# Optimization experiments

Hardware: AMD Instinct MI355X
Metric: run time of the kernel (lower is better)

The kernel has to match this reference:

```python
import jax, jax.numpy as jnp
import numpy as np

N = 50000      # num_nodes
R = 90         # num_relations
E = 800000     # num_edges
H = 16         # hidden channels
B = 30         # num_bases
C = 8          # num_classes


def setup_inputs() -> dict:
    key = jax.random.key(0)
    ks = jax.random.split(key, 10)
    edge_index = jax.random.randint(ks[0], (2, E), 0, N, dtype=jnp.int64)
    edge_type = jax.random.randint(ks[1], (E,), 0, R, dtype=jnp.int64)
    s1 = 1.0 / np.sqrt(N)
    s2 = 1.0 / np.sqrt(H)
    return {
        "edge_index": edge_index,
        "edge_type": edge_type,
        # layer 1: in=N (featureless one-hot), out=H
        "basis1": jax.random.normal(ks[2], (B, N, H), jnp.float32) * s1,
        "comp1": jax.random.normal(ks[3], (R, B), jnp.float32) * (1.0 / np.sqrt(B)),
        "root1": jax.random.normal(ks[4], (N, H), jnp.float32) * s1,
        "bias1": jnp.zeros((H,), jnp.float32),
        # layer 2: in=H, out=C
        "basis2": jax.random.normal(ks[5], (B, H, C), jnp.float32) * s2,
        "comp2": jax.random.normal(ks[6], (R, B), jnp.float32) * (1.0 / np.sqrt(B)),
        "root2": jax.random.normal(ks[7], (H, C), jnp.float32) * s2,
        "bias2": jnp.zeros((C,), jnp.float32),
    }


def reference(edge_index, edge_type, basis1, comp1, root1, bias1,
              basis2, comp2, root2, bias2):
    src, dst = edge_index[0], edge_index[1]
    # per-(dst, relation) degree -> mean aggregation per relation (PyG RGCNConv aggr='mean')
    seg = dst * R + edge_type                      # [E]
    deg = jax.ops.segment_sum(jnp.ones((E,), jnp.float32), seg, num_segments=N * R)
    inv_deg = jnp.where(deg > 0, 1.0 / jnp.maximum(deg, 1.0), 0.0)
    norm = inv_deg[seg][:, None]                   # [E, 1]

    # ---- layer 1 (x = None -> one-hot node features; message = W_r[src]) ----
    W1 = jnp.einsum('rb,bnh->rnh', comp1, basis1)  # [R, N, H]
    m1 = W1[edge_type, src] * norm                 # [E, H]
    h = jax.ops.segment_sum(m1, dst, num_segments=N) + root1 + bias1  # [N, H]
    h = jax.nn.relu(h)

    # ---- layer 2 ----
    W2 = jnp.einsum('rb,bhc->rhc', comp2, basis2)  # [R, H, C]
    m2 = jnp.einsum('eh,ehc->ec', h[src], W2[edge_type]) * norm       # [E, C]
    out = jax.ops.segment_sum(m2, dst, num_segments=N) + h @ root2 + bias2
    return jax.nn.log_softmax(out, axis=1)
```

## Files before the change

### kernel.cpp

```cpp
#include <hip/hip_runtime.h>

#define NNODES 50000
#define NREL   90
#define NEDGE  800000
#define HDIM   16
#define NBASIS 30
#define NCLS   8
#define NPART  392
#define CH     2048
#define P1BLK  ((NEDGE + CH - 1) / CH)
#define CAPSTG 2816
#define GS     8
#define BSTR2  260
#define CROW2  20

typedef __fp16 h2 __attribute__((ext_vector_type(2)));

static __device__ __forceinline__ unsigned pk2(float a, float b) {
    h2 p = __builtin_amdgcn_cvt_pkrtz(a, b);
    return __builtin_bit_cast(unsigned, p);
}
static __device__ __forceinline__ h2 uph(unsigned u) {
    return __builtin_bit_cast(h2, u);
}
static __device__ __forceinline__ float fd2(unsigned a, unsigned b, float c) {
#if __has_builtin(__builtin_amdgcn_fdot2)
    return __builtin_amdgcn_fdot2(uph(a), uph(b), c, false);
#else
    h2 x = uph(a), y = uph(b);
    return fmaf((float)x.y, (float)y.y, fmaf((float)x.x, (float)y.x, c));
#endif
}

__device__ __forceinline__ void scan512_incl(int* sc) {
    int t = threadIdx.x;
#pragma unroll
    for (int d = 1; d < 512; d <<= 1) {
        int v0 = sc[t];
        int a0 = (t >= d) ? sc[t - d] : 0;
        int v1 = sc[t + 256];
        int a1 = sc[t + 256 - d];
        __syncthreads();
        sc[t] = v0 + a0;
        sc[t + 256] = v1 + a1;
        __syncthreads();
    }
}

__device__ __forceinline__ void scan128_incl(int* sc) {
    int t = threadIdx.x;
#pragma unroll
    for (int d = 1; d < 128; d <<= 1) {
        int v = 0, a = 0;
        if (t < 128) { v = sc[t]; a = (t >= d) ? sc[t - d] : 0; }
        __syncthreads();
        if (t < 128) sc[t] = v + a;
        __syncthreads();
    }
}

__global__ __launch_bounds__(256) void initc_kernel(int* __restrict__ gcur_s,
                                                    int* __restrict__ gcur_d,
                                                    int* __restrict__ gcnt,
                                                    const float* __restrict__ comp1,
                                                    unsigned* __restrict__ comp_pk) {
    int t = blockIdx.x * 256 + threadIdx.x;
    if (t < NPART) { gcur_s[t] = t * CAPSTG; gcur_d[t] = t * CAPSTG; }
    else if (t == NPART) { gcnt[0] = 0; gcnt[1] = 0; }
    int i = t - 512;
    if (i >= 0 && i < NREL * 15) {
        int r = i / 15;
        int b2 = i - r * 15;
        comp_pk[r * CROW2 + b2] = pk2(comp1[r * NBASIS + 2 * b2],
                                      comp1[r * NBASIS + 2 * b2 + 1]);
    }
    if (i >= NREL * 15 && i < NREL * 15 + NREL * (CROW2 - 15)) {
        int j = i - NREL * 15;
        int r = j / (CROW2 - 15);
        int pcol = 15 + (j - r * (CROW2 - 15));
        comp_pk[r * CROW2 + pcol] = 0;
    }
}

__global__ __launch_bounds__(256) void p1d_kernel(const int* __restrict__ ei,
                                                  const int* __restrict__ et,
                                                  int* __restrict__ gcur_d,
                                                  int2* __restrict__ stg_d) {
    __shared__ int2 sorted[CH];
    __shared__ int hist[NPART], loff[NPART], cur[NPART], gbase[NPART];
    __shared__ int sc[512];
    int base = blockIdx.x * CH;
    int nitems = min(CH, NEDGE - base);
    int t = threadIdx.x;
    for (int i = t; i < NPART; i += 256) hist[i] = 0;
    __syncthreads();
    for (int i = t; i < nitems; i += 256)
        atomicAdd(&hist[ei[NEDGE + base + i] >> 7], 1);
    __syncthreads();
    sc[t]       = (t < NPART) ? hist[t] : 0;
    sc[t + 256] = (t + 256 < NPART) ? hist[t + 256] : 0;
    __syncthreads();
    scan512_incl(sc);
    for (int p = t; p < NPART; p += 256) {
        int lo = p ? sc[p - 1] : 0;
        loff[p] = lo;
        cur[p] = lo;
        if (hist[p]) gbase[p] = atomicAdd(&gcur_d[p], hist[p]);
    }
    __syncthreads();
    for (int i = t; i < nitems; i += 256) {
        int e = base + i;
        int src = ei[e], dst = ei[NEDGE + e], r = et[e];
        int rk = atomicAdd(&cur[dst >> 7], 1);
        sorted[rk] = make_int2(src | (r << 16), dst);
    }
    __syncthreads();
    for (int s = t; s < nitems; s += 256) {
        int2 it = sorted[s];
        int p = it.y >> 7;
        stg_d[gbase[p] + (s - loff[p])] = it;
    }
}

__global__ __launch_bounds__(256) void p2d_kernel(const int* __restrict__ gcur_d,
                                                  const int2* __restrict__ stg_d,
                                                  int* __restrict__ gcur_s,
                                                  int2* __restrict__ stg_s,
                                                  int* __restrict__ gcnt,
                                                  int* __restrict__ d_sr,
                                                  float* __restrict__ d_norm,
                                                  int* __restrict__ offs_d,
                                                  int* __restrict__ cnt_d) {
    __shared__ int2 sorted[CAPSTG];
    __shared__ int2 sorted2[CAPSTG];
    __shared__ int h[128], off[128], cur[128];
    __shared__ int sc[512];
    __shared__ int shist[NPART], sloff[NPART], scur[NPART], sgbase[NPART];
    __shared__ int kb;
    int p = blockIdx.x;
    int base = p * CAPSTG;
    int n = min(gcur_d[p] - base, CAPSTG);
    int t = threadIdx.x;
    if (t < 128) h[t] = 0;
    __syncthreads();
    for (int s = t; s < n; s += 256)
        atomicAdd(&h[stg_d[base + s].y & 127], 1);
    __syncthreads();
    if (t < 128) sc[t] = h[t];
    __syncthreads();
    scan128_incl(sc);
    if (t < 128) { int lo = t ? sc[t - 1] : 0; off[t] = lo; cur[t] = lo; }
    if (t == 0) kb = atomicAdd(&gcnt[0], n);
    __syncthreads();
    for (int s = t; s < n; s += 256) {
        int2 it = stg_d[base + s];
        int rk = atomicAdd(&cur[it.y & 127], 1);
        sorted[rk] = it;
    }
    __syncthreads();
    int kbase = kb;
    for (int s = t; s < n; s += 256) {
        int2 it = sorted[s];
        int key = it.y & 127;
        int r = it.x >> 16;
        int o = off[key], oe = o + h[key];
        int c = 0;
        for (int kk = o; kk < oe; ++kk)
            c += ((sorted[kk].x >> 16) == r);
        d_sr[kbase + s] = it.x;
        d_norm[kbase + s] = 1.0f / (float)c;
    }
    if (t < 128) {
        int node = (p << 7) + t;
        if (node < NNODES) { offs_d[node] = kbase + off[t]; cnt_d[node] = h[t]; }
    }
    for (int i = t; i < NPART; i += 256) shist[i] = 0;
    __syncthreads();
    for (int s = t; s < n; s += 256)
        atomicAdd(&shist[(sorted[s].x & 0xFFFF) >> 7], 1);
    __syncthreads();
    sc[t]       = (t < NPART) ? shist[t] : 0;
    sc[t + 256] = (t + 256 < NPART) ? shist[t + 256] : 0;
    __syncthreads();
    scan512_incl(sc);
    for (int pp = t; pp < NPART; pp += 256) {
        int lo = pp ? sc[pp - 1] : 0;
        sloff[pp] = lo;
        scur[pp] = lo;
        if (shist[pp]) sgbase[pp] = atomicAdd(&gcur_s[pp], shist[pp]);
    }
    __syncthreads();
    for (int s = t; s < n; s += 256) {
        int2 it = sorted[s];
        int rk = atomicAdd(&scur[(it.x & 0xFFFF) >> 7], 1);
        sorted2[rk] = make_int2(it.x, kbase + s);
    }
    __syncthreads();
    for (int s = t; s < n; s += 256) {
        int2 it = sorted2[s];
        int pp = (it.x & 0xFFFF) >> 7;
        stg_s[sgbase[pp] + (s - sloff[pp])] = it;
    }
}

__global__ __launch_bounds__(256) void p2s_kernel(const int* __restrict__ gcur_s,
                                                  const int2* __restrict__ stg_s,
                                                  int* __restrict__ gcnt,
                                                  int* __restrict__ sB,
                                                  int* __restrict__ s_k,
                                                  int* __restrict__ offs_s,
                                                  int* __restrict__ cnt_s) {
    __shared__ int2 sorted[CAPSTG];
    __shared__ int h[128], off[128], cur[128], sc[128];
    __shared__ int jb;
    int p = blockIdx.x;
    int base = p * CAPSTG;
    int n = min(gcur_s[p] - base, CAPSTG);
    int t = threadIdx.x;
    if (t < 128) h[t] = 0;
    __syncthreads();
    for (int s = t; s < n; s += 256)
        atomicAdd(&h[stg_s[base + s].x & 127], 1);
    __syncthreads();
    if (t < 128) sc[t] = h[t];
    __syncthreads();
    scan128_incl(sc);
    if (t < 128) { int lo = t ? sc[t - 1] : 0; off[t] = lo; cur[t] = lo; }
    if (t == 0) jb = atomicAdd(&gcnt[1], n);
    __syncthreads();
    for (int s = t; s < n; s += 256) {
        int2 it = stg_s[base + s];
        int rk = atomicAdd(&cur[it.x & 127], 1);
        sorted[rk] = it;
    }
    __syncthreads();
    int jbase = jb;
    for (int s = t; s < n; s += 256) {
        int2 it = sorted[s];
        sB[jbase + s]  = it.x;
        s_k[jbase + s] = it.y;
    }
    if (t < 128) {
        int node = (p << 7) + t;
        if (node < NNODES) { offs_s[node] = jbase + off[t]; cnt_s[node] = h[t]; }
    }
}

__global__ __launch_bounds__(256) void msg1_lds(const float* __restrict__ basis1,
                                                const unsigned* __restrict__ comp_pk,
                                                const int* __restrict__ offs_s,
                                                const int* __restrict__ cnt_s,
                                                const int* __restrict__ sB,
                                                const int* __restrict__ s_k,
                                                unsigned* __restrict__ m1) {
    __shared__ unsigned bspk[GS * BSTR2];
    __shared__ unsigned cpk[NREL * CROW2];
    int src0 = blockIdx.x * GS;
    int t = threadIdx.x;
    for (int i = t; i < (NREL * CROW2) / 4; i += 256)
        ((uint4*)cpk)[i] = ((const uint4*)comp_pk)[i];
    for (int i4 = t; i4 < 15 * 32; i4 += 256) {
        int b2 = i4 >> 5;
        int w  = i4 & 31;
        const float4* bp = (const float4*)basis1;
        float4 a = bp[(size_t)(2 * b2)     * (NNODES * 4) + (size_t)src0 * 4 + w];
        float4 b = bp[(size_t)(2 * b2 + 1) * (NNODES * 4) + (size_t)src0 * 4 + w];
        int s = w >> 2, q = w & 3;
        uint4 o;
        o.x = pk2(a.x, b.x);
        o.y = pk2(a.y, b.y);
        o.z = pk2(a.z, b.z);
        o.w = pk2(a.w, b.w);
        *((uint4*)(bspk + s * BSTR2 + b2 * 16 + q * 4)) = o;
    }
    __syncthreads();
    int n0 = offs_s[src0];
    int lastS = src0 + GS - 1;
    int n1 = offs_s[lastS] + cnt_s[lastS];
    for (int ii = n0 * 4 + t; ii < n1 * 4; ii += 256) {
        int j = ii >> 2;
        int q = ii & 3;
        int pk = sB[j];
        int k  = s_k[j];
        int src = pk & 0xFFFF;
        int r   = pk >> 16;
        const uint4* crow = (const uint4*)(cpk + r * CROW2);
        uint4 c0 = crow[0], c1 = crow[1], c2 = crow[2], c3 = crow[3];
        const unsigned* bw = bspk + (src - src0) * BSTR2 + q * 4;
        float a0 = 0.f, a1 = 0.f, a2 = 0.f, a3 = 0.f;
#define MSG1_STEP(B2, CB) { \
        uint4 v = *((const uint4*)(bw + (B2) * 16)); \
        a0 = fd2(v.x, (CB), a0); \
        a1 = fd2(v.y, (CB), a1); \
        a2 = fd2(v.z, (CB), a2); \
        a3 = fd2(v.w, (CB), a3); }
        MSG1_STEP(0,  c0.x) MSG1_STEP(1,  c0.y) MSG1_STEP(2,  c0.z) MSG1_STEP(3,  c0.w)
        MSG1_STEP(4,  c1.x) MSG1_STEP(5,  c1.y) MSG1_STEP(6,  c1.z) MSG1_STEP(7,  c1.w)
        MSG1_STEP(8,  c2.x) MSG1_STEP(9,  c2.y) MSG1_STEP(10, c2.z) MSG1_STEP(11, c2.w)
        MSG1_STEP(12, c3.x) MSG1_STEP(13, c3.y) MSG1_STEP(14, c3.z)
#undef MSG1_STEP
        ((uint2*)m1)[(size_t)k * 4 + q] = make_uint2(pk2(a0, a1), pk2(a2, a3));
    }
}

__global__ __launch_bounds__(256) void gather1_flat(const unsigned* __restrict__ m1,
                                                    const float* __restrict__ d_norm,
                                                    const int* __restrict__ offs_d,
                                                    const int* __restrict__ cnt_d,
                                                    const float* __restrict__ root1,
                                                    const float* __restrict__ bias1,
                                                    float* __restrict__ h,
                                                    unsigned* __restrict__ h16) {
    int idx = blockIdx.x * blockDim.x + threadIdx.x;
    if (idx >= NNODES * 4) return;
    int dst = idx >> 2;
    int q   = idx & 3;
    int k0 = offs_d[dst];
    int k1 = k0 + cnt_d[dst];
    float4 acc = make_float4(0.f, 0.f, 0.f, 0.f);
    for (int k = k0; k < k1; ++k) {
        uint2 v = ((const uint2*)m1)[(size_t)k * 4 + q];
        float nm = d_norm[k];
        h2 x = uph(v.x), y = uph(v.y);
        acc.x = fmaf(nm, (float)x.x, acc.x);
        acc.y = fmaf(nm, (float)x.y, acc.y);
        acc.z = fmaf(nm, (float)y.x, acc.z);
        acc.w = fmaf(nm, (float)y.y, acc.w);
    }
    float4 rt = ((const float4*)root1)[idx];
    float4 bi = ((const float4*)bias1)[q];
    float4 o;
    o.x = fmaxf(acc.x + rt.x + bi.x, 0.f);
    o.y = fmaxf(acc.y + rt.y + bi.y, 0.f);
    o.z = fmaxf(acc.z + rt.z + bi.z, 0.f);
    o.w = fmaxf(acc.w + rt.w + bi.w, 0.f);
    ((float4*)h)[idx] = o;
    ((uint2*)h16)[idx] = make_uint2(pk2(o.x, o.y), pk2(o.z, o.w));
}

__global__ __launch_bounds__(256) void w2pk_kernel(const float* __restrict__ basis2,
                                                   const float* __restrict__ comp2,
                                                   const float* __restrict__ root2,
                                                   unsigned* __restrict__ w2pk,
                                                   float* __restrict__ r2t) {
    int i = blockIdx.x * blockDim.x + threadIdx.x;
    if (i >= NREL * NCLS * 8) return;
    int r = i >> 6;
    int c = (i >> 3) & (NCLS - 1);
    int p = i & 7;
    float a0 = 0.f, a1 = 0.f;
#pragma unroll
    for (int b = 0; b < NBASIS; ++b) {
        float cb = comp2[r * NBASIS + b];
        a0 = fmaf(cb, basis2[(b * HDIM + 2 * p)     * NCLS + c], a0);
        a1 = fmaf(cb, basis2[(b * HDIM + 2 * p + 1) * NCLS + c], a1);
    }
    w2pk[i] = pk2(a0, a1);
    if (i < HDIM * NCLS) {
        int c2 = i >> 4;
        int k2 = i & (HDIM - 1);
        r2t[i] = root2[k2 * NCLS + c2];
    }
}

__global__ __launch_bounds__(256) void msg2_kernel(const unsigned* __restrict__ h16,
                                                   const unsigned* __restrict__ w2pk,
                                                   const int* __restrict__ d_sr,
                                                   const float* __restrict__ d_norm,
                                                   float* __restrict__ m2) {
    int idx = blockIdx.x * blockDim.x + threadIdx.x;
    int k = idx >> 3;
    int c = idx & (NCLS - 1);
    int pk = d_sr[k];
    float nm = d_norm[k];
    int src = pk & 0xFFFF;
    int r   = pk >> 16;
    const uint4* __restrict__ hp = (const uint4*)(h16 + src * 8);
    const uint4* __restrict__ wp = (const uint4*)(w2pk + (r * NCLS + c) * 8);
    uint4 h0 = hp[0], h1 = hp[1];
    uint4 w0 = wp[0], w1 = wp[1];
    float a = 0.f;
    a = fd2(h0.x, w0.x, a);
    a = fd2(h0.y, w0.y, a);
    a = fd2(h0.z, w0.z, a);
    a = fd2(h0.w, w0.w, a);
    a = fd2(h1.x, w1.x, a);
    a = fd2(h1.y, w1.y, a);
    a = fd2(h1.z, w1.z, a);
    a = fd2(h1.w, w1.w, a);
    m2[idx] = nm * a;
}

__global__ __launch_bounds__(256) void gather2_kernel(const float* __restrict__ m2,
                                                      const float* __restrict__ h,
                                                      const float* __restrict__ r2t,
                                                      const int* __restrict__ offs_d,
                                                      const int* __restrict__ cnt_d,
                                                      const float* __restrict__ bias2,
                                                      float* __restrict__ out) {
    int idx = blockIdx.x * blockDim.x + threadIdx.x;
    if (idx >= NNODES * NCLS) return;
    int dst = idx >> 3;
    int c   = idx & (NCLS - 1);
    int k0 = offs_d[dst];
    int k1 = k0 + cnt_d[dst];
    float acc = 0.f;
    for (int k = k0; k < k1; ++k)
        acc += m2[k * NCLS + c];
    float v = acc + bias2[c];
    const float4* __restrict__ hd = (const float4*)h + dst * 4;
    const float4* __restrict__ rp = (const float4*)r2t + c * 4;
#pragma unroll
    for (int qq = 0; qq < 4; ++qq) {
        float4 hv = hd[qq];
        float4 rv = rp[qq];
        v = fmaf(hv.x, rv.x, v);
        v = fmaf(hv.y, rv.y, v);
        v = fmaf(hv.z, rv.z, v);
        v = fmaf(hv.w, rv.w, v);
    }
    float mx = v;
    mx = fmaxf(mx, __shfl_xor(mx, 1));
    mx = fmaxf(mx, __shfl_xor(mx, 2));
    mx = fmaxf(mx, __shfl_xor(mx, 4));
    float s = expf(v - mx);
    s += __shfl_xor(s, 1);
    s += __shfl_xor(s, 2);
    s += __shfl_xor(s, 4);
    out[idx] = v - mx - logf(s);
}

__global__ __launch_bounds__(256) void degcnt_fb(const int* __restrict__ ei,
                                                 const int* __restrict__ et,
                                                 int* __restrict__ deg) {
    int e = blockIdx.x * blockDim.x + threadIdx.x;
    if (e >= NEDGE) return;
    atomicAdd(&deg[ei[NEDGE + e] * NREL + et[e]], 1);
}

__global__ __launch_bounds__(256) void layer1_flat(const int* __restrict__ ei,
                                                   const int* __restrict__ et,
                                                   const float* __restrict__ basis1,
                                                   const float* __restrict__ comp1,
                                                   const int* __restrict__ deg,
                                                   float* __restrict__ h) {
    long long idx = (long long)blockIdx.x * blockDim.x + threadIdx.x;
    if (idx >= (long long)NEDGE * HDIM) return;
    int e  = (int)(idx >> 4);
    int hh = (int)(idx & (HDIM - 1));
    int src = ei[e];
    int dst = ei[NEDGE + e];
    int r   = et[e];
    float norm = 1.0f / (float)deg[dst * NREL + r];
    const float* __restrict__ cp = comp1 + r * NBASIS;
    float acc = 0.f;
#pragma unroll
    for (int b = 0; b < NBASIS; ++b)
        acc += cp[b] * basis1[(b * NNODES + src) * HDIM + hh];
    atomicAdd(&h[dst * HDIM + hh], norm * acc);
}

__global__ __launch_bounds__(256) void relu_kernel(float* __restrict__ h,
                                                   const float* __restrict__ root1,
                                                   const float* __restrict__ bias1) {
    int i = blockIdx.x * blockDim.x + threadIdx.x;
    if (i >= NNODES * HDIM) return;
    float v = h[i] + root1[i] + bias1[i & (HDIM - 1)];
    h[i] = v > 0.f ? v : 0.f;
}

__global__ __launch_bounds__(256) void w2_kernel_fb(const float* __restrict__ basis2,
                                                    const float* __restrict__ comp2,
                                                    const float* __restrict__ root2,
                                                    float* __restrict__ w2t,
                                                    float* __restrict__ r2t) {
    int i = blockIdx.x * blockDim.x + threadIdx.x;
    if (i >= NREL * HDIM * NCLS) return;
    int kk = i & (HDIM - 1);
    int c  = (i >> 4) & (NCLS - 1);
    int r  = i >> 7;
    float acc = 0.f;
#pragma unroll
    for (int b = 0; b < NBASIS; ++b)
        acc += comp2[r * NBASIS + b] * basis2[(b * HDIM + kk) * NCLS + c];
    w2t[i] = acc;
    if (i < HDIM * NCLS) {
        int c2 = i >> 4;
        int k2 = i & (HDIM - 1);
        r2t[i] = root2[k2 * NCLS + c2];
    }
}

__global__ __launch_bounds__(256) void layer2_flat(const int* __restrict__ ei,
                                                   const int* __restrict__ et,
                                                   const float* __restrict__ h,
                                                   const float* __restrict__ w2t,
                                                   const int* __restrict__ deg,
                                                   float* __restrict__ out_tmp) {
    long long idx = (long long)blockIdx.x * blockDim.x + threadIdx.x;
    if (idx >= (long long)NEDGE * NCLS) return;
    int e = (int)(idx >> 3);
    int c = (int)(idx & (NCLS - 1));
    int src = ei[e];
    int dst = ei[NEDGE + e];
    int r   = et[e];
    float norm = 1.0f / (float)deg[dst * NREL + r];
    const float4* __restrict__ hp = (const float4*)h + src * 4;
    const float4* __restrict__ wp = (const float4*)w2t + (r * NCLS + c) * 4;
    float a = 0.f;
#pragma unroll
    for (int qq = 0; qq < 4; ++qq) {
        float4 hv = hp[qq];
        float4 wv = wp[qq];
        a = fmaf(hv.x, wv.x, a);
        a = fmaf(hv.y, wv.y, a);
        a = fmaf(hv.z, wv.z, a);
        a = fmaf(hv.w, wv.w, a);
    }
    atomicAdd(&out_tmp[dst * NCLS + c], norm * a);
}

__global__ __launch_bounds__(256) void final_kernel(const float* __restrict__ out_tmp,
                                                    const float* __restrict__ h,
                                                    const float* __restrict__ root2,
                                                    const float* __restrict__ bias2,
                                                    float* __restrict__ out) {
    int n = blockIdx.x * blockDim.x + threadIdx.x;
    if (n >= NNODES) return;
    float hv[HDIM];
#pragma unroll
    for (int i = 0; i < HDIM; ++i) hv[i] = h[n * HDIM + i];
    float v[NCLS];
    float mx = -1e30f;
#pragma unroll
    for (int c = 0; c < NCLS; ++c) {
        float acc = out_tmp[n * NCLS + c] + bias2[c];
#pragma unroll
        for (int i = 0; i < HDIM; ++i) acc += hv[i] * root2[i * NCLS + c];
        v[c] = acc;
        mx = fmaxf(mx, acc);
    }
    float s = 0.f;
#pragma unroll
    for (int c = 0; c < NCLS; ++c) s += expf(v[c] - mx);
    float ls = logf(s);
#pragma unroll
    for (int c = 0; c < NCLS; ++c) out[n * NCLS + c] = v[c] - mx - ls;
}

extern "C" void kernel_launch(void* const* d_in, const int* in_sizes, int n_in,
                              void* d_out, int out_size, void* d_ws, size_t ws_size,
                              hipStream_t stream) {
    const int*   ei     = (const int*)d_in[0];
    const int*   et     = (const int*)d_in[1];
    const float* basis1 = (const float*)d_in[2];
    const float* comp1  = (const float*)d_in[3];
    const float* root1  = (const float*)d_in[4];
    const float* bias1  = (const float*)d_in[5];
    const float* basis2 = (const float*)d_in[6];
    const float* comp2  = (const float*)d_in[7];
    const float* root2  = (const float*)d_in[8];
    const float* bias2  = (const float*)d_in[9];
    float* out = (float*)d_out;

    int*      gcur_s  = (int*)d_ws;
    int*      gcur_d  = gcur_s + NPART;
    int*      gcnt    = gcur_d + NPART;
    unsigned* comp_pk = (unsigned*)(gcnt + 4);
    int2*  stg_d  = (int2*)(comp_pk + NREL * CROW2);
    int2*  stg_s  = stg_d + (size_t)NPART * CAPSTG;
    int*   d_sr   = (int*)(stg_s + (size_t)NPART * CAPSTG);
    float* d_norm = (float*)(d_sr + NEDGE);
    int*   sB     = (int*)(d_norm + NEDGE);
    int*   s_k    = sB + NEDGE;
    int*   offs_s = s_k + NEDGE;
    int*   cnt_s  = offs_s + NNODES;
    int*   offs_d = cnt_s + NNODES;
    int*   cnt_d  = offs_d + NNODES;
    unsigned* m1  = (unsigned*)(cnt_d + NNODES);
    float* m2     = (float*)m1;
    float* h      = (float*)(m1 + (size_t)NEDGE * 8);
    unsigned* h16 = (unsigned*)(h + (size_t)NNODES * HDIM);
    unsigned* w2pk = h16 + (size_t)NNODES * 8;
    float* r2t    = (float*)(w2pk + (size_t)NREL * NCLS * 8);
    size_t total_words = 2 * (size_t)NPART + 4 + NREL * CROW2 +
                         4 * (size_t)NPART * CAPSTG +
                         4 * (size_t)NEDGE + 4 * (size_t)NNODES +
                         (size_t)NEDGE * 8 + (size_t)NNODES * HDIM +
                         (size_t)NNODES * 8 + (size_t)NREL * NCLS * 8 + HDIM * NCLS;

    if (ws_size >= total_words * sizeof(float)) {
        initc_kernel<<<8, 256, 0, stream>>>(gcur_s, gcur_d, gcnt, comp1, comp_pk);
        p1d_kernel<<<P1BLK, 256, 0, stream>>>(ei, et, gcur_d, stg_d);
        p2d_kernel<<<NPART - 1, 256, 0, stream>>>(gcur_d, stg_d, gcur_s, stg_s, gcnt,
                                                  d_sr, d_norm, offs_d, cnt_d);
        p2s_kernel<<<NPART - 1, 256, 0, stream>>>(gcur_s, stg_s, gcnt, sB, s_k, offs_s, cnt_s);

        msg1_lds<<<NNODES / GS, 256, 0, stream>>>(basis1, comp_pk, offs_s, cnt_s, sB, s_k, m1);
        gather1_flat<<<(NNODES * 4 + 255) / 256, 256, 0, stream>>>(
            m1, d_norm, offs_d, cnt_d, root1, bias1, h, h16);
        w2pk_kernel<<<(NREL * NCLS * 8 + 255) / 256, 256, 0, stream>>>(basis2, comp2, root2,
                                                                       w2pk, r2t);
        msg2_kernel<<<(NEDGE * NCLS) / 256, 256, 0, stream>>>(h16, w2pk, d_sr, d_norm, m2);
        gather2_kernel<<<(NNODES * NCLS + 255) / 256, 256, 0, stream>>>(
            m2, h, r2t, offs_d, cnt_d, bias2, out);
        return;
    }

    {
        int*   deg_f   = (int*)d_ws;
        float* h_f     = (float*)(deg_f + (size_t)NNODES * NREL);
        float* out_tmp = h_f + (size_t)NNODES * HDIM;
        size_t zw = (size_t)NNODES * NREL + NNODES * HDIM + NNODES * NCLS;
        float* w2t_f   = out_tmp + (size_t)NNODES * NCLS;
        float* r2t_f   = w2t_f + (size_t)NREL * HDIM * NCLS;

        (void)hipMemsetAsync(d_ws, 0, zw * sizeof(float), stream);
        degcnt_fb<<<(NEDGE + 255) / 256, 256, 0, stream>>>(ei, et, deg_f);
        layer1_flat<<<((size_t)NEDGE * HDIM + 255) / 256, 256, 0, stream>>>(
            ei, et, basis1, comp1, deg_f, h_f);
        relu_kernel<<<(NNODES * HDIM + 255) / 256, 256, 0, stream>>>(h_f, root1, bias1);
        w2_kernel_fb<<<(NREL * HDIM * NCLS + 255) / 256, 256, 0, stream>>>(basis2, comp2, root2,
                                                                           w2t_f, r2t_f);
        layer2_flat<<<((size_t)NEDGE * NCLS + 255) / 256, 256, 0, stream>>>(
            ei, et, h_f, w2t_f, deg_f, out_tmp);
        final_kernel<<<(NNODES + 255) / 256, 256, 0, stream>>>(out_tmp, h_f, root2, bias2, out);
    }
}
```

Measured before the change: 155.2 us.

## Sort edges by source first, then destination, writing layer-1 messages contiguously

The two-pass partition sort now orders edges by source first and by destination second. msg1 can then write its per-edge messages in source-sorted order, no longer scattering through a permutation index, and gather1 reads them indirectly through a new d_j index. This moves the random access from msg1's writes to gather1's reads and drops the s_k array. Relation, source and local destination bits are packed into one word, which limits the value ranges it can hold.

```diff
diff --git a/kernel.cpp b/kernel.cpp
--- a/kernel.cpp
+++ b/kernel.cpp
@@ -82,10 +82,10 @@
     }
 }
 
-__global__ __launch_bounds__(256) void p1d_kernel(const int* __restrict__ ei,
+__global__ __launch_bounds__(256) void p1s_kernel(const int* __restrict__ ei,
                                                   const int* __restrict__ et,
-                                                  int* __restrict__ gcur_d,
-                                                  int2* __restrict__ stg_d) {
+                                                  int* __restrict__ gcur_s,
+                                                  int2* __restrict__ stg_s) {
     __shared__ int2 sorted[CH];
     __shared__ int hist[NPART], loff[NPART], cur[NPART], gbase[NPART];
     __shared__ int sc[512];
@@ -95,7 +95,7 @@
     for (int i = t; i < NPART; i += 256) hist[i] = 0;
     __syncthreads();
     for (int i = t; i < nitems; i += 256)
-        atomicAdd(&hist[ei[NEDGE + base + i] >> 7], 1);
+        atomicAdd(&hist[ei[base + i] >> 7], 1);
     __syncthreads();
     sc[t]       = (t < NPART) ? hist[t] : 0;
     sc[t + 256] = (t + 256 < NPART) ? hist[t + 256] : 0;
@@ -105,37 +105,112 @@
         int lo = p ? sc[p - 1] : 0;
         loff[p] = lo;
         cur[p] = lo;
-        if (hist[p]) gbase[p] = atomicAdd(&gcur_d[p], hist[p]);
+        if (hist[p]) gbase[p] = atomicAdd(&gcur_s[p], hist[p]);
     }
     __syncthreads();
     for (int i = t; i < nitems; i += 256) {
         int e = base + i;
         int src = ei[e], dst = ei[NEDGE + e], r = et[e];
-        int rk = atomicAdd(&cur[dst >> 7], 1);
-        sorted[rk] = make_int2(src | (r << 16), dst);
+        int rk = atomicAdd(&cur[src >> 7], 1);
+        sorted[rk] = make_int2(dst | (r << 16), src);
     }
     __syncthreads();
     for (int s = t; s < nitems; s += 256) {
         int2 it = sorted[s];
         int p = it.y >> 7;
-        stg_d[gbase[p] + (s - loff[p])] = it;
-    }
-}
-
-__global__ __launch_bounds__(256) void p2d_kernel(const int* __restrict__ gcur_d,
-                                                  const int2* __restrict__ stg_d,
-                                                  int* __restrict__ gcur_s,
-                                                  int2* __restrict__ stg_s,
+        stg_s[gbase[p] + (s - loff[p])] = it;
+    }
+}
+
+__global__ __launch_bounds__(256) void p2s_kernel(const int* __restrict__ gcur_s,
+                                                  const int2* __restrict__ stg_s,
+                                                  int* __restrict__ gcur_d,
+                                                  int2* __restrict__ stg_d,
                                                   int* __restrict__ gcnt,
-                                                  int* __restrict__ d_sr,
-                                                  float* __restrict__ d_norm,
-                                                  int* __restrict__ offs_d,
-                                                  int* __restrict__ cnt_d) {
+                                                  int* __restrict__ sB,
+                                                  int* __restrict__ offs_s,
+                                                  int* __restrict__ cnt_s) {
     __shared__ int2 sorted[CAPSTG];
     __shared__ int2 sorted2[CAPSTG];
     __shared__ int h[128], off[128], cur[128];
     __shared__ int sc[512];
     __shared__ int shist[NPART], sloff[NPART], scur[NPART], sgbase[NPART];
+    __shared__ int jb;
+    int p = blockIdx.x;
+    int base = p * CAPSTG;
+    int n = min(gcur_s[p] - base, CAPSTG);
+    int t = threadIdx.x;
+    if (t < 128) h[t] = 0;
+    __syncthreads();
+    for (int s = t; s < n; s += 256)
+        atomicAdd(&h[stg_s[base + s].y & 127], 1);
+    __syncthreads();
+    if (t < 128) sc[t] = h[t];
+    __syncthreads();
+    scan128_incl(sc);
+    if (t < 128) { int lo = t ? sc[t - 1] : 0; off[t] = lo; cur[t] = lo; }
+    if (t == 0) jb = atomicAdd(&gcnt[1], n);
+    __syncthreads();
+    for (int s = t; s < n; s += 256) {
+        int2 it = stg_s[base + s];
+        int rk = atomicAdd(&cur[it.y & 127], 1);
+        sorted[rk] = it;
+    }
+    __syncthreads();
+    int jbase = jb;
+    for (int s = t; s < n; s += 256) {
+        int2 it = sorted[s];
+        int r = it.x >> 16;
+        sB[jbase + s] = it.y | (r << 16);
+    }
+    if (t < 128) {
+        int node = (p << 7) + t;
+        if (node < NNODES) { offs_s[node] = jbase + off[t]; cnt_s[node] = h[t]; }
+    }
+    for (int i = t; i < NPART; i += 256) shist[i] = 0;
+    __syncthreads();
+    for (int s = t; s < n; s += 256)
+        atomicAdd(&shist[(sorted[s].x & 0xFFFF) >> 7], 1);
+    __syncthreads();
+    sc[t]       = (t < NPART) ? shist[t] : 0;
+    sc[t + 256] = (t + 256 < NPART) ? shist[t + 256] : 0;
+    __syncthreads();
+    scan512_incl(sc);
+    for (int pp = t; pp < NPART; pp += 256) {
+        int lo = pp ? sc[pp - 1] : 0;
+        sloff[pp] = lo;
+        scur[pp] = lo;
+        if (shist[pp]) sgbase[pp] = atomicAdd(&gcur_d[pp], shist[pp]);
+    }
+    __syncthreads();
+    for (int s = t; s < n; s += 256) {
+        int2 it = sorted[s];
+        int dst = it.x & 0xFFFF;
+        int r   = it.x >> 16;
+        int src = it.y;
+        int pp  = dst >> 7;
+        int rk = atomicAdd(&scur[pp], 1);
+        sorted2[rk] = make_int2(src | (r << 16) | ((dst & 127) << 23),
+                                (jbase + s) | (pp << 20));
+    }
+    __syncthreads();
+    for (int s = t; s < n; s += 256) {
+        int2 it = sorted2[s];
+        int pp = ((unsigned)it.y) >> 20;
+        stg_d[sgbase[pp] + (s - sloff[pp])] = make_int2(it.x, it.y & 0xFFFFF);
+    }
+}
+
+__global__ __launch_bounds__(256) void p2d_kernel(const int* __restrict__ gcur_d,
+                                                  const int2* __restrict__ stg_d,
+                                                  int* __restrict__ gcnt,
+                                                  int* __restrict__ d_sr,
+                                                  int* __restrict__ d_j,
+                                                  float* __restrict__ d_norm,
+                                                  int* __restrict__ offs_d,
+                                                  int* __restrict__ cnt_d) {
+    __shared__ int2 sorted[CAPSTG];
+    __shared__ int h[128], off[128], cur[128], sc[128];
     __shared__ int kb;
     int p = blockIdx.x;
     int base = p * CAPSTG;
@@ -144,7 +219,7 @@
     if (t < 128) h[t] = 0;
     __syncthreads();
     for (int s = t; s < n; s += 256)
-        atomicAdd(&h[stg_d[base + s].y & 127], 1);
+        atomicAdd(&h[(stg_d[base + s].x >> 23) & 127], 1);
     __syncthreads();
     if (t < 128) sc[t] = h[t];
     __syncthreads();
@@ -154,95 +229,26 @@
     __syncthreads();
     for (int s = t; s < n; s += 256) {
         int2 it = stg_d[base + s];
-        int rk = atomicAdd(&cur[it.y & 127], 1);
+        int rk = atomicAdd(&cur[(it.x >> 23) & 127], 1);
         sorted[rk] = it;
     }
     __syncthreads();
     int kbase = kb;
     for (int s = t; s < n; s += 256) {
         int2 it = sorted[s];
-        int key = it.y & 127;
-        int r = it.x >> 16;
+        int key = (it.x >> 23) & 127;
+        int r = (it.x >> 16) & 127;
         int o = off[key], oe = o + h[key];
         int c = 0;
         for (int kk = o; kk < oe; ++kk)
-            c += ((sorted[kk].x >> 16) == r);
-        d_sr[kbase + s] = it.x;
+            c += (((sorted[kk].x >> 16) & 127) == r);
+        d_sr[kbase + s]   = it.x & 0x7FFFFF;
+        d_j[kbase + s]    = it.y;
         d_norm[kbase + s] = 1.0f / (float)c;
     }
     if (t < 128) {
         int node = (p << 7) + t;
         if (node < NNODES) { offs_d[node] = kbase + off[t]; cnt_d[node] = h[t]; }
-    }
-    for (int i = t; i < NPART; i += 256) shist[i] = 0;
-    __syncthreads();
-    for (int s = t; s < n; s += 256)
-        atomicAdd(&shist[(sorted[s].x & 0xFFFF) >> 7], 1);
-    __syncthreads();
-    sc[t]       = (t < NPART) ? shist[t] : 0;
-    sc[t + 256] = (t + 256 < NPART) ? shist[t + 256] : 0;
-    __syncthreads();
-    scan512_incl(sc);
-    for (int pp = t; pp < NPART; pp += 256) {
-        int lo = pp ? sc[pp - 1] : 0;
-        sloff[pp] = lo;
-        scur[pp] = lo;
-        if (shist[pp]) sgbase[pp] = atomicAdd(&gcur_s[pp], shist[pp]);
-    }
-    __syncthreads();
-    for (int s = t; s < n; s += 256) {
-        int2 it = sorted[s];
-        int rk = atomicAdd(&scur[(it.x & 0xFFFF) >> 7], 1);
-        sorted2[rk] = make_int2(it.x, kbase + s);
-    }
-    __syncthreads();
-    for (int s = t; s < n; s += 256) {
-        int2 it = sorted2[s];
-        int pp = (it.x & 0xFFFF) >> 7;
-        stg_s[sgbase[pp] + (s - sloff[pp])] = it;
-    }
-}
-
-__global__ __launch_bounds__(256) void p2s_kernel(const int* __restrict__ gcur_s,
-                                                  const int2* __restrict__ stg_s,
-                                                  int* __restrict__ gcnt,
-                                                  int* __restrict__ sB,
-                                                  int* __restrict__ s_k,
-                                                  int* __restrict__ offs_s,
-                                                  int* __restrict__ cnt_s) {
-    __shared__ int2 sorted[CAPSTG];
-    __shared__ int h[128], off[128], cur[128], sc[128];
-    __shared__ int jb;
-    int p = blockIdx.x;
-    int base = p * CAPSTG;
-    int n = min(gcur_s[p] - base, CAPSTG);
-    int t = threadIdx.x;
-    if (t < 128) h[t] = 0;
-    __syncthreads();
-    for (int s = t; s < n; s += 256)
-        atomicAdd(&h[stg_s[base + s].x & 127], 1);
-    __syncthreads();
-    if (t < 128) sc[t] = h[t];
-    __syncthreads();
-    scan128_incl(sc);
-    if (t < 128) { int lo = t ? sc[t - 1] : 0; off[t] = lo; cur[t] = lo; }
-    if (t == 0) jb = atomicAdd(&gcnt[1], n);
-    __syncthreads();
-    for (int s = t; s < n; s += 256) {
-        int2 it = stg_s[base + s];
-        int rk = atomicAdd(&cur[it.x & 127], 1);
-        sorted[rk] = it;
-    }
-    __syncthreads();
-    int jbase = jb;
-    for (int s = t; s < n; s += 256) {
-        int2 it = sorted[s];
-        sB[jbase + s]  = it.x;
-        s_k[jbase + s] = it.y;
-    }
-    if (t < 128) {
-        int node = (p << 7) + t;
-        if (node < NNODES) { offs_s[node] = jbase + off[t]; cnt_s[node] = h[t]; }
     }
 }
 
@@ -251,7 +257,6 @@
                                                 const int* __restrict__ offs_s,
                                                 const int* __restrict__ cnt_s,
                                                 const int* __restrict__ sB,
-                                                const int* __restrict__ s_k,
                                                 unsigned* __restrict__ m1) {
     __shared__ unsigned bspk[GS * BSTR2];
     __shared__ unsigned cpk[NREL * CROW2];
@@ -281,7 +286,6 @@
         int j = ii >> 2;
         int q = ii & 3;
         int pk = sB[j];
-        int k  = s_k[j];
         int src = pk & 0xFFFF;
         int r   = pk >> 16;
         const uint4* crow = (const uint4*)(cpk + r * CROW2);
@@ -299,11 +303,12 @@
         MSG1_STEP(8,  c2.x) MSG1_STEP(9,  c2.y) MSG1_STEP(10, c2.z) MSG1_STEP(11, c2.w)
         MSG1_STEP(12, c3.x) MSG1_STEP(13, c3.y) MSG1_STEP(14, c3.z)
 #undef MSG1_STEP
-        ((uint2*)m1)[(size_t)k * 4 + q] = make_uint2(pk2(a0, a1), pk2(a2, a3));
+        ((uint2*)m1)[(size_t)j * 4 + q] = make_uint2(pk2(a0, a1), pk2(a2, a3));
     }
 }
 
 __global__ __launch_bounds__(256) void gather1_flat(const unsigned* __restrict__ m1,
+                                                    const int* __restrict__ d_j,
                                                     const float* __restrict__ d_norm,
                                                     const int* __restrict__ offs_d,
                                                     const int* __restrict__ cnt_d,
@@ -319,7 +324,8 @@
     int k1 = k0 + cnt_d[dst];
     float4 acc = make_float4(0.f, 0.f, 0.f, 0.f);
     for (int k = k0; k < k1; ++k) {
-        uint2 v = ((const uint2*)m1)[(size_t)k * 4 + q];
+        int j = d_j[k];
+        uint2 v = ((const uint2*)m1)[(size_t)j * 4 + q];
         float nm = d_norm[k];
         h2 x = uph(v.x), y = uph(v.y);
         acc.x = fmaf(nm, (float)x.x, acc.x);
@@ -567,13 +573,13 @@
     int*      gcur_d  = gcur_s + NPART;
     int*      gcnt    = gcur_d + NPART;
     unsigned* comp_pk = (unsigned*)(gcnt + 4);
-    int2*  stg_d  = (int2*)(comp_pk + NREL * CROW2);
-    int2*  stg_s  = stg_d + (size_t)NPART * CAPSTG;
-    int*   d_sr   = (int*)(stg_s + (size_t)NPART * CAPSTG);
+    int2*  stg_s  = (int2*)(comp_pk + NREL * CROW2);
+    int2*  stg_d  = stg_s + (size_t)NPART * CAPSTG;
+    int*   d_sr   = (int*)(stg_d + (size_t)NPART * CAPSTG);
     float* d_norm = (float*)(d_sr + NEDGE);
     int*   sB     = (int*)(d_norm + NEDGE);
-    int*   s_k    = sB + NEDGE;
-    int*   offs_s = s_k + NEDGE;
+    int*   d_j    = sB + NEDGE;
+    int*   offs_s = d_j + NEDGE;
     int*   cnt_s  = offs_s + NNODES;
     int*   offs_d = cnt_s + NNODES;
     int*   cnt_d  = offs_d + NNODES;
@@ -591,14 +597,15 @@
 
     if (ws_size >= total_words * sizeof(float)) {
         initc_kernel<<<8, 256, 0, stream>>>(gcur_s, gcur_d, gcnt, comp1, comp_pk);
-        p1d_kernel<<<P1BLK, 256, 0, stream>>>(ei, et, gcur_d, stg_d);
-        p2d_kernel<<<NPART - 1, 256, 0, stream>>>(gcur_d, stg_d, gcur_s, stg_s, gcnt,
-                                                  d_sr, d_norm, offs_d, cnt_d);
-        p2s_kernel<<<NPART - 1, 256, 0, stream>>>(gcur_s, stg_s, gcnt, sB, s_k, offs_s, cnt_s);
-
-        msg1_lds<<<NNODES / GS, 256, 0, stream>>>(basis1, comp_pk, offs_s, cnt_s, sB, s_k, m1);
+        p1s_kernel<<<P1BLK, 256, 0, stream>>>(ei, et, gcur_s, stg_s);
+        p2s_kernel<<<NPART - 1, 256, 0, stream>>>(gcur_s, stg_s, gcur_d, stg_d, gcnt,
+                                                  sB, offs_s, cnt_s);
+        p2d_kernel<<<NPART - 1, 256, 0, stream>>>(gcur_d, stg_d, gcnt,
+                                                  d_sr, d_j, d_norm, offs_d, cnt_d);
+
+        msg1_lds<<<NNODES / GS, 256, 0, stream>>>(basis1, comp_pk, offs_s, cnt_s, sB, m1);
         gather1_flat<<<(NNODES * 4 + 255) / 256, 256, 0, stream>>>(
-            m1, d_norm, offs_d, cnt_d, root1, bias1, h, h16);
+            m1, d_j, d_norm, offs_d, cnt_d, root1, bias1, h, h16);
         w2pk_kernel<<<(NREL * NCLS * 8 + 255) / 256, 256, 0, stream>>>(basis2, comp2, root2,
                                                                        w2pk, r2t);
         msg2_kernel<<<(NEDGE * NCLS) / 256, 256, 0, stream>>>(h16, w2pk, d_sr, d_norm, m2);
```

After: 160.8 us. 3.6% more time.
